# Kernel tuning notes

Hardware: AMD Instinct MI355X
Metric: run time of the kernel (lower is better)

## Reference

```python
import jax, jax.numpy as jnp
import numpy as np

NHEAD = 16
HEAD_DIM = 64
ROPE_BASE = 10000.0


def _rotate_half(x):
    # interleaved convention: pairs (x0,x1)->(-x1,x0)
    x1 = x[..., ::2]
    x2 = x[..., 1::2]
    return jnp.stack([-x2, x1], axis=-1).reshape(x.shape)


def _rope_cache(seq_len, head_dim, base):
    half = head_dim // 2
    inv_freq = 1.0 / base ** (jnp.arange(half, dtype=jnp.float32) / float(half))
    t = jnp.arange(seq_len, dtype=jnp.float32)
    freqs = jnp.einsum('i,j->ij', t, inv_freq)          # [T, half]
    emb = jnp.concatenate([freqs, freqs], axis=-1)      # [T, D] (half-half cat, matches torch source)
    return jnp.cos(emb), jnp.sin(emb)


def setup_inputs() -> dict:
    key = jax.random.key(0)
    k1, k2, k3 = jax.random.split(key, 3)
    b, t, c = 2, 2048, 1024
    x = jax.random.normal(k1, (b, t, c), dtype=jnp.float32)
    # torch nn.Linear weights: [out_features, in_features], scaled like kaiming-uniform-ish
    W_qkv = jax.random.normal(k2, (3 * c, c), dtype=jnp.float32) / np.sqrt(c)
    W_out = jax.random.normal(k3, (c, c), dtype=jnp.float32) / np.sqrt(c)
    return {"x": x, "W_qkv": W_qkv, "W_out": W_out}


def reference(x, W_qkv, W_out):
    b, t, c = x.shape
    nh, hd = NHEAD, HEAD_DIM
    qkv = x @ W_qkv.T                                   # [b, t, 3c]
    q, k, v = jnp.split(qkv, 3, axis=-1)

    def to_heads(a):
        return a.reshape(b, t, nh, hd).transpose(0, 2, 1, 3)  # [b, nh, t, hd]

    q, k, v = to_heads(q), to_heads(k), to_heads(v)
    cos, sin = _rope_cache(t, hd, ROPE_BASE)            # [t, hd]
    cos = cos.astype(q.dtype)[None, None]
    sin = sin.astype(q.dtype)[None, None]
    q = q * cos + _rotate_half(q) * sin
    k = k * cos + _rotate_half(k) * sin

    scale = 1.0 / np.sqrt(hd).astype(np.float32)
    scores = jnp.einsum('bhqd,bhkd->bhqk', q, k) * scale
    attn = jax.nn.softmax(scores, axis=-1)
    y = jnp.einsum('bhqk,bhkd->bhqd', attn, v)          # [b, nh, t, hd]
    y = y.transpose(0, 2, 1, 3).reshape(b, t, c)
    return y @ W_out.T
```

## Files before the change

kernel.cpp:

```cpp
#include <hip/hip_runtime.h>
#include <hip/hip_bf16.h>
#include <math.h>

typedef __hip_bfloat16 bf16;
typedef _Float16 f16;
typedef __attribute__((ext_vector_type(8))) short bf16x8;
typedef __attribute__((ext_vector_type(8))) _Float16 f16x8;
typedef __attribute__((ext_vector_type(4))) float f32x4;
typedef __attribute__((ext_vector_type(4))) unsigned u32x4;

#define MFMA_BF(a,b,c) __builtin_amdgcn_mfma_f32_16x16x32_bf16((a),(b),(c),0,0,0)
#define MFMA_F16(a,b,c) __builtin_amdgcn_mfma_f32_16x16x32_f16((a),(b),(c),0,0,0)

__device__ __forceinline__ void load_lds16(const void* g, void* l) {
  __builtin_amdgcn_global_load_lds(
      (__attribute__((address_space(1))) void*)(g),
      (__attribute__((address_space(3))) void*)(l), 16, 0, 0);
}

__device__ __forceinline__ unsigned pk_bf16(float a, float b) {
  unsigned ua = __builtin_bit_cast(unsigned, a);
  unsigned ub = __builtin_bit_cast(unsigned, b);
  ua += 0x7fffu + ((ua >> 16) & 1u);
  ub += 0x7fffu + ((ub >> 16) & 1u);
  return (ua >> 16) | (ub & 0xffff0000u);
}

__global__ void cvt_all(const float* __restrict__ x, const float* __restrict__ wq,
                        const float* __restrict__ wo, unsigned* __restrict__ xb,
                        unsigned* __restrict__ wqb, unsigned* __restrict__ wob) {
  int i = blockIdx.x * blockDim.x + threadIdx.x;
  const float* src;
  unsigned* dst;
  int off;
  if (i < 1048576) { src = x; dst = xb; off = i; }
  else if (i < 1048576 + 786432) { src = wq; dst = wqb; off = i - 1048576; }
  else { src = wo; dst = wob; off = i - (1048576 + 786432); }
  float4 v = reinterpret_cast<const float4*>(src)[off];
  uint2 u;
  u.x = pk_bf16(v.x, v.y);
  u.y = pk_bf16(v.z, v.w);
  reinterpret_cast<uint2*>(dst)[off] = u;
}

__global__ __launch_bounds__(256, 2)
void gemm_qkv(const bf16* __restrict__ A, const bf16* __restrict__ B,
              bf16* __restrict__ outq, bf16* __restrict__ outk,
              f16* __restrict__ outv) {
  __shared__ __align__(16) bf16 As[3][128 * 32];
  __shared__ __align__(16) bf16 Bs[3][128 * 32];
  const int K = 1024;
  const int tid = threadIdx.x;
  const int w = tid >> 6;
  const int lane = tid & 63;
  const int quad = lane >> 4;
  const int col = lane & 15;
  const int waveM = w >> 1;
  const int waveN = w & 1;
  const int bm = blockIdx.y * 128;
  const int bn = blockIdx.x * 128;

  f32x4 acc[4][4] = {};
  const int srow = lane >> 2;
  const int skoff = (((lane & 3) ^ ((srow >> 1) & 3))) * 8;
  const int swq = (quad ^ ((col >> 1) & 3)) * 8;

  auto stage = [&](int k0, int sb) {
#pragma unroll
    for (int p = 0; p < 2; ++p) {
      int r = p * 64 + w * 16 + srow;
      load_lds16(A + (size_t)(bm + r) * K + k0 + skoff,
                 (char*)As + sb * 8192 + p * 4096 + w * 1024);
      load_lds16(B + (size_t)(bn + r) * K + k0 + skoff,
                 (char*)Bs + sb * 8192 + p * 4096 + w * 1024);
    }
  };

  stage(0, 0);
  stage(32, 1);

  int cb = 0;
  for (int k0 = 0; k0 < K; k0 += 32) {
    if (k0 + 32 < K) __asm__ volatile("s_waitcnt vmcnt(4)" ::: "memory");
    else             __asm__ volatile("s_waitcnt vmcnt(0)" ::: "memory");
    __asm__ volatile("s_barrier" ::: "memory");
    if (k0 + 64 < K) {
      int nb = cb + 2; if (nb >= 3) nb -= 3;
      stage(k0 + 64, nb);
    }
    const bf16* at = &As[cb][0];
    const bf16* bt = &Bs[cb][0];
    bf16x8 af[4], bfr[4];
#pragma unroll
    for (int i = 0; i < 4; ++i)
      af[i] = *reinterpret_cast<const bf16x8*>(at + (waveM * 64 + i * 16 + col) * 32 + swq);
#pragma unroll
    for (int j = 0; j < 4; ++j)
      bfr[j] = *reinterpret_cast<const bf16x8*>(bt + (waveN * 64 + j * 16 + col) * 32 + swq);
#pragma unroll
    for (int i = 0; i < 4; ++i)
#pragma unroll
      for (int j = 0; j < 4; ++j)
        acc[i][j] = MFMA_BF(af[i], bfr[j], acc[i][j]);
    cb = (cb == 2) ? 0 : cb + 1;
  }

  if (bn < 2048) {
    const float NEGK = -0.4152410118f;
    const float C1 = 0.1803368799f;
    const float sgn = (col & 1) ? 1.0f : -1.0f;
#pragma unroll
    for (int j = 0; j < 4; ++j) {
      const int n0 = bn + waveN * 64 + j * 16;
      const int sel = n0 >> 10;
      const int hh = (n0 & 1023) >> 6;
      const int dd = (n0 & 63) + col;
      bf16* outp = sel ? outk : outq;
      const float post = sel ? 1.0f : C1;
      const float invf = __builtin_amdgcn_exp2f((float)((n0 & 31) + col) * NEGK);
#pragma unroll
      for (int i = 0; i < 4; ++i) {
#pragma unroll
        for (int r = 0; r < 4; ++r) {
          int m = bm + waveM * 64 + i * 16 + quad * 4 + r;
          int b = m >> 11, t = m & 2047;
          float v = acc[i][j][r];
          float partner = __shfl_xor(v, 1);
          float ang = (float)t * invf;
          float res = (v * __cosf(ang) + sgn * partner * __sinf(ang)) * post;
          outp[((size_t)(b * 16 + hh) * 2048 + t) * 64 + dd] = __float2bfloat16(res);
        }
      }
    }
  } else {
    const int b = bm >> 11;
    const int tt0 = (bm & 2047) + waveM * 64;
#pragma unroll
    for (int j = 0; j < 4; ++j) {
      const int n0 = bn + waveN * 64 + j * 16;
      const int hh = (n0 & 1023) >> 6;
      const int dd = (n0 & 63) + col;
      f16* dst = outv + (size_t)(b * 16 + hh) * 131072 + (size_t)dd * 2048;
#pragma unroll
      for (int i = 0; i < 4; ++i) {
        uint2 pk;
        pk.x = __builtin_bit_cast(unsigned, __builtin_amdgcn_cvt_pkrtz(acc[i][j][0], acc[i][j][1]));
        pk.y = __builtin_bit_cast(unsigned, __builtin_amdgcn_cvt_pkrtz(acc[i][j][2], acc[i][j][3]));
        *reinterpret_cast<uint2*>(dst + tt0 + i * 16 + quad * 4) = pk;
      }
    }
  }
}

__global__ __launch_bounds__(256, 2)
void gemm_out(const bf16* __restrict__ A, const bf16* __restrict__ B,
              float* __restrict__ outf) {
  __shared__ __align__(16) bf16 As[3][64 * 32];
  __shared__ __align__(16) bf16 Bs[3][128 * 32];
  const int K = 1024;
  const int tid = threadIdx.x;
  const int w = tid >> 6;
  const int lane = tid & 63;
  const int quad = lane >> 4;
  const int col = lane & 15;
  const int bm = blockIdx.y * 64;
  const int bn = blockIdx.x * 128;

  f32x4 acc[4][2] = {};
  const int srow = lane >> 2;
  const int skoff = (((lane & 3) ^ ((srow >> 1) & 3))) * 8;
  const int swq = (quad ^ ((col >> 1) & 3)) * 8;

  auto stage = [&](int k0, int sb) {
    load_lds16(A + (size_t)(bm + w * 16 + srow) * K + k0 + skoff,
               (char*)As + sb * 4096 + w * 1024);
#pragma unroll
    for (int p = 0; p < 2; ++p)
      load_lds16(B + (size_t)(bn + p * 64 + w * 16 + srow) * K + k0 + skoff,
                 (char*)Bs + sb * 8192 + p * 4096 + w * 1024);
  };

  stage(0, 0);
  stage(32, 1);

  int cb = 0;
  for (int k0 = 0; k0 < K; k0 += 32) {
    if (k0 + 32 < K) __asm__ volatile("s_waitcnt vmcnt(3)" ::: "memory");
    else             __asm__ volatile("s_waitcnt vmcnt(0)" ::: "memory");
    __asm__ volatile("s_barrier" ::: "memory");
    if (k0 + 64 < K) {
      int nb = cb + 2; if (nb >= 3) nb -= 3;
      stage(k0 + 64, nb);
    }
    const bf16* at = &As[cb][0];
    const bf16* bt = &Bs[cb][0];
    bf16x8 af[4], bfr[2];
#pragma unroll
    for (int i = 0; i < 4; ++i)
      af[i] = *reinterpret_cast<const bf16x8*>(at + (i * 16 + col) * 32 + swq);
#pragma unroll
    for (int j = 0; j < 2; ++j)
      bfr[j] = *reinterpret_cast<const bf16x8*>(bt + (w * 32 + j * 16 + col) * 32 + swq);
#pragma unroll
    for (int i = 0; i < 4; ++i)
#pragma unroll
      for (int j = 0; j < 2; ++j)
        acc[i][j] = MFMA_BF(af[i], bfr[j], acc[i][j]);
    cb = (cb == 2) ? 0 : cb + 1;
  }

#pragma unroll
  for (int i = 0; i < 4; ++i)
#pragma unroll
    for (int j = 0; j < 2; ++j) {
      const int n0 = bn + w * 32 + j * 16;
#pragma unroll
      for (int r = 0; r < 4; ++r) {
        int m = bm + i * 16 + quad * 4 + r;
        outf[(size_t)m * 1024 + n0 + col] = acc[i][j][r];
      }
    }
}

__global__ __launch_bounds__(256, 2)
void attn_kernel(const bf16* __restrict__ qh, const bf16* __restrict__ kh,
                 const f16* __restrict__ vt, bf16* __restrict__ y) {
  __shared__ __align__(16) bf16 Ks[3][64 * 64];
  __shared__ __align__(16) f16 Vs[3][64 * 64];

  const int bh = blockIdx.y;
  const int w = threadIdx.x >> 6;
  const int lane = threadIdx.x & 63;
  const int quad = lane >> 4;
  const int col = lane & 15;
  const int kg = w & 1;
  const int qg = w >> 1;

  const int qbase = blockIdx.x * 128 + qg * 64 + col;
  bf16x8 qf[4][2];
#pragma unroll
  for (int f = 0; f < 4; ++f)
#pragma unroll
    for (int c = 0; c < 2; ++c)
      qf[f][c] = *reinterpret_cast<const bf16x8*>(
          qh + ((size_t)bh * 2048 + qbase + f * 16) * 64 + c * 32 + quad * 8);

  const int s8 = lane >> 3;
  const int blk = (lane & 7) ^ s8;
  const bf16* kg_ptr = kh + (size_t)bh * 2048 * 64;
  const f16* vg_ptr = vt + (size_t)bh * 64 * 2048;
  const int ks0 = (w >> 1) * 32 + (w & 1) * 4 + 8 * (s8 >> 2) + (s8 & 3);
  const int ks1 = ks0 + 16;
  const int vrow0 = w * 16 + s8;

  const int csw = col & 7;
  const int sw0 = (quad ^ csw) * 8;
  const int sw1 = ((quad + 4) ^ csw) * 8;
  const int vsw = ((kg * 4 + quad) ^ csw) * 8;
  const int krow = kg * 32;

  f32x4 O[4][4] = {};
  float l[4] = {};

  auto stage = [&](int kn, int sb) {
    char* kb = (char*)Ks + sb * 8192 + w * 2048;
    char* vb = (char*)Vs + sb * 8192 + w * 2048;
    load_lds16(kg_ptr + (size_t)(kn + ks0) * 64 + blk * 8, kb);
    load_lds16(kg_ptr + (size_t)(kn + ks1) * 64 + blk * 8, kb + 1024);
    load_lds16(vg_ptr + (size_t)vrow0 * 2048 + kn + blk * 8, vb);
    load_lds16(vg_ptr + (size_t)(vrow0 + 8) * 2048 + kn + blk * 8, vb + 1024);
  };

  stage(0, 0);
  stage(64, 1);

  int cb = 0;
  for (int kc = 0; kc < 2048; kc += 64) {
    if (kc + 64 < 2048) __asm__ volatile("s_waitcnt vmcnt(4)" ::: "memory");
    else                __asm__ volatile("s_waitcnt vmcnt(0)" ::: "memory");
    __asm__ volatile("s_barrier" ::: "memory");
    if (kc + 128 < 2048) {
      int nb = cb + 2; if (nb >= 3) nb -= 3;
      stage(kc + 128, nb);
    }

    const bf16* kt_p = &Ks[cb][0];
    const f16* vtile = &Vs[cb][0];

    bf16x8 kf[2][2];
#pragma unroll
    for (int t = 0; t < 2; ++t) {
      kf[t][0] = *reinterpret_cast<const bf16x8*>(kt_p + (krow + t * 16 + col) * 64 + sw0);
      kf[t][1] = *reinterpret_cast<const bf16x8*>(kt_p + (krow + t * 16 + col) * 64 + sw1);
    }

    f32x4 s[2][4];
#pragma unroll
    for (int t = 0; t < 2; ++t)
#pragma unroll
      for (int f = 0; f < 4; ++f) {
        f32x4 a = {};
        a = MFMA_BF(kf[t][0], qf[f][0], a);
        a = MFMA_BF(kf[t][1], qf[f][1], a);
        s[t][f] = a;
      }

    f16x8 pf[4];
#pragma unroll
    for (int f = 0; f < 4; ++f) {
      float p00 = __builtin_amdgcn_exp2f(s[0][f][0]);
      float p01 = __builtin_amdgcn_exp2f(s[0][f][1]);
      float p02 = __builtin_amdgcn_exp2f(s[0][f][2]);
      float p03 = __builtin_amdgcn_exp2f(s[0][f][3]);
      float p10 = __builtin_amdgcn_exp2f(s[1][f][0]);
      float p11 = __builtin_amdgcn_exp2f(s[1][f][1]);
      float p12 = __builtin_amdgcn_exp2f(s[1][f][2]);
      float p13 = __builtin_amdgcn_exp2f(s[1][f][3]);
      l[f] += ((p00 + p01) + (p02 + p03)) + ((p10 + p11) + (p12 + p13));
      u32x4 pk;
      pk.x = __builtin_bit_cast(unsigned, __builtin_amdgcn_cvt_pkrtz(p00, p01));
      pk.y = __builtin_bit_cast(unsigned, __builtin_amdgcn_cvt_pkrtz(p02, p03));
      pk.z = __builtin_bit_cast(unsigned, __builtin_amdgcn_cvt_pkrtz(p10, p11));
      pk.w = __builtin_bit_cast(unsigned, __builtin_amdgcn_cvt_pkrtz(p12, p13));
      pf[f] = __builtin_bit_cast(f16x8, pk);
    }

#pragma unroll
    for (int jt = 0; jt < 4; ++jt) {
      f16x8 vf = *reinterpret_cast<const f16x8*>(vtile + (jt * 16 + col) * 64 + vsw);
#pragma unroll
      for (int f = 0; f < 4; ++f)
        O[jt][f] = MFMA_F16(vf, pf[f], O[jt][f]);
    }
    cb = (cb == 2) ? 0 : cb + 1;
  }

#pragma unroll
  for (int f = 0; f < 4; ++f) {
    l[f] += __shfl_xor(l[f], 16, 64);
    l[f] += __shfl_xor(l[f], 32, 64);
  }

  float* xb = (float*)&Ks[0][0];
  if (kg == 1) {
    float* dst = xb + qg * 4352 + lane * 68;
#pragma unroll
    for (int jt = 0; jt < 4; ++jt)
#pragma unroll
      for (int f = 0; f < 4; ++f)
        *reinterpret_cast<f32x4*>(dst + (jt * 4 + f) * 4) = O[jt][f];
#pragma unroll
    for (int f = 0; f < 4; ++f) dst[64 + f] = l[f];
  }
  __syncthreads();
  if (kg == 0) {
    const float* src = xb + qg * 4352 + lane * 68;
    const int b = bh >> 4, h = bh & 15;
#pragma unroll
    for (int f = 0; f < 4; ++f) {
      float lv = l[f] + src[64 + f];
      float inv = 1.0f / lv;
      int q = qbase - col + f * 16 + col;
      size_t base = ((size_t)b * 2048 + q) * 1024 + h * 64;
#pragma unroll
      for (int jt = 0; jt < 4; ++jt) {
        f32x4 o = O[jt][f] + *reinterpret_cast<const f32x4*>(src + (jt * 4 + f) * 4);
        uint2 pk2;
        pk2.x = pk_bf16(o[0] * inv, o[1] * inv);
        pk2.y = pk_bf16(o[2] * inv, o[3] * inv);
        *reinterpret_cast<uint2*>((unsigned short*)y + base + jt * 16 + quad * 4) = pk2;
      }
    }
  }
}

extern "C" void kernel_launch(void* const* d_in, const int* in_sizes, int n_in,
                              void* d_out, int out_size, void* d_ws, size_t ws_size,
                              hipStream_t stream) {
  const float* x    = (const float*)d_in[0];
  const float* wqkv = (const float*)d_in[1];
  const float* wout = (const float*)d_in[2];
  float* out = (float*)d_out;
  char* ws = (char*)d_ws;

  bf16* xb    = (bf16*)(ws);
  bf16* wqkvb = (bf16*)(ws + (size_t)(8 << 20));
  bf16* woutb = (bf16*)(ws + (size_t)(14 << 20));
  bf16* qh    = (bf16*)(ws + (size_t)(16 << 20));
  bf16* kh    = (bf16*)(ws + (size_t)(24 << 20));
  f16*  vt    = (f16*) (ws + (size_t)(32 << 20));
  bf16* y     = (bf16*)(ws + (size_t)(40 << 20));

  cvt_all<<<8192, 256, 0, stream>>>(x, wqkv, wout,
                                    (unsigned*)xb, (unsigned*)wqkvb, (unsigned*)woutb);
  gemm_qkv<<<dim3(24, 32), 256, 0, stream>>>(xb, wqkvb, qh, kh, vt);
  attn_kernel<<<dim3(16, 32), 256, 0, stream>>>(qh, kh, vt, y);
  gemm_out<<<dim3(8, 64), 256, 0, stream>>>(y, woutb, out);
}
```

Before: 178.8 us.

## Software-pipeline attention loop: compute next QK^T while doing current PV

The attention inner loop is restructured so the QK^T MFMAs for the next key tile are issued in the same iteration as the PV MFMAs for the current tile, with exp/pack of the current scores done first. The LDS ring buffer grows from 3 to 4 stages so K for tile i+1 and V for tile i stay resident while tile i+3 is prefetched. This aims to hide exp latency and LDS reads behind independent MFMA work. In exchange it uses more LDS (64KB per block), which may reduce occupancy at 2 blocks per CU, and it adds a final __syncthreads before the LDS reuse in the epilogue.

```diff
diff --git a/kernel.cpp b/kernel.cpp
--- a/kernel.cpp
+++ b/kernel.cpp
@@ -225,8 +225,8 @@
 __global__ __launch_bounds__(256, 2)
 void attn_kernel(const bf16* __restrict__ qh, const bf16* __restrict__ kh,
                  const f16* __restrict__ vt, bf16* __restrict__ y) {
-  __shared__ __align__(16) bf16 Ks[3][64 * 64];
-  __shared__ __align__(16) f16 Vs[3][64 * 64];
+  __shared__ __align__(16) bf16 Ks[4][64 * 64];
+  __shared__ __align__(16) f16 Vs[4][64 * 64];
 
   const int bh = blockIdx.y;
   const int w = threadIdx.x >> 6;
@@ -273,28 +273,19 @@
 
   stage(0, 0);
   stage(64, 1);
-
-  int cb = 0;
-  for (int kc = 0; kc < 2048; kc += 64) {
-    if (kc + 64 < 2048) __asm__ volatile("s_waitcnt vmcnt(4)" ::: "memory");
-    else                __asm__ volatile("s_waitcnt vmcnt(0)" ::: "memory");
-    __asm__ volatile("s_barrier" ::: "memory");
-    if (kc + 128 < 2048) {
-      int nb = cb + 2; if (nb >= 3) nb -= 3;
-      stage(kc + 128, nb);
-    }
-
-    const bf16* kt_p = &Ks[cb][0];
-    const f16* vtile = &Vs[cb][0];
-
+  stage(128, 2);
+  __asm__ volatile("s_waitcnt vmcnt(8)" ::: "memory");
+  __asm__ volatile("s_barrier" ::: "memory");
+
+  f32x4 s[2][4];
+  {
+    const bf16* kt_p = &Ks[0][0];
     bf16x8 kf[2][2];
 #pragma unroll
     for (int t = 0; t < 2; ++t) {
       kf[t][0] = *reinterpret_cast<const bf16x8*>(kt_p + (krow + t * 16 + col) * 64 + sw0);
       kf[t][1] = *reinterpret_cast<const bf16x8*>(kt_p + (krow + t * 16 + col) * 64 + sw1);
     }
-
-    f32x4 s[2][4];
 #pragma unroll
     for (int t = 0; t < 2; ++t)
 #pragma unroll
@@ -304,7 +295,9 @@
         a = MFMA_BF(kf[t][1], qf[f][1], a);
         s[t][f] = a;
       }
-
+  }
+
+  for (int i = 0; i < 32; ++i) {
     f16x8 pf[4];
 #pragma unroll
     for (int f = 0; f < 4; ++f) {
@@ -325,6 +318,32 @@
       pf[f] = __builtin_bit_cast(f16x8, pk);
     }
 
+    if (i < 30) __asm__ volatile("s_waitcnt vmcnt(4)" ::: "memory");
+    else        __asm__ volatile("s_waitcnt vmcnt(0)" ::: "memory");
+    __asm__ volatile("s_barrier" ::: "memory");
+    if (i < 29) stage((i + 3) * 64, (i + 3) & 3);
+
+    const f16* vtile = &Vs[i & 3][0];
+
+    if (i < 31) {
+      const bf16* kt_p = &Ks[(i + 1) & 3][0];
+      bf16x8 kf[2][2];
+#pragma unroll
+      for (int t = 0; t < 2; ++t) {
+        kf[t][0] = *reinterpret_cast<const bf16x8*>(kt_p + (krow + t * 16 + col) * 64 + sw0);
+        kf[t][1] = *reinterpret_cast<const bf16x8*>(kt_p + (krow + t * 16 + col) * 64 + sw1);
+      }
+#pragma unroll
+      for (int t = 0; t < 2; ++t)
+#pragma unroll
+        for (int f = 0; f < 4; ++f) {
+          f32x4 a = {};
+          a = MFMA_BF(kf[t][0], qf[f][0], a);
+          a = MFMA_BF(kf[t][1], qf[f][1], a);
+          s[t][f] = a;
+        }
+    }
+
 #pragma unroll
     for (int jt = 0; jt < 4; ++jt) {
       f16x8 vf = *reinterpret_cast<const f16x8*>(vtile + (jt * 16 + col) * 64 + vsw);
@@ -332,7 +351,6 @@
       for (int f = 0; f < 4; ++f)
         O[jt][f] = MFMA_F16(vf, pf[f], O[jt][f]);
     }
-    cb = (cb == 2) ? 0 : cb + 1;
   }
 
 #pragma unroll
@@ -341,6 +359,7 @@
     l[f] += __shfl_xor(l[f], 32, 64);
   }
 
+  __syncthreads();
   float* xb = (float*)&Ks[0][0];
   if (kg == 1) {
     float* dst = xb + qg * 4352 + lane * 68;
@@ -360,7 +379,7 @@
     for (int f = 0; f < 4; ++f) {
       float lv = l[f] + src[64 + f];
       float inv = 1.0f / lv;
-      int q = qbase - col + f * 16 + col;
+      int q = qbase + f * 16;
       size_t base = ((size_t)b * 2048 + q) * 1024 + h * 64;
 #pragma unroll
       for (int jt = 0; jt < 4; ++jt) {
```

New measurement: 179.3 us. Within noise of the previous version (+0.3%).
